# Optimization experiments

Hardware: AMD Instinct MI355X
Metric: run time of the kernel (lower is better)

## Reference

```python
import jax, jax.numpy as jnp
import numpy as np

OBS = 256      # observation_space_size == state_vector_len
SV = 2047      # STATE_VECTORS = WMG_MAX_OBS
D = 256        # tfm_vec_size = 8 heads * 32 head_size
H = 8
HD = 32
L = 2          # TFM_NUM_LAYERS
FF = 1024      # TFM_HIDDEN_SIZE
ACH = 512      # AC_HIDDEN_LAYER_SIZE
A = 16         # action_space_size


def setup_inputs() -> dict:
    key = jax.random.key(0)
    ks = jax.random.split(key, 24)
    r = lambda k, s: (jax.random.normal(k, s, jnp.float32) * 0.02)
    inp = {
        "observation": jax.random.normal(ks[0], (OBS,), jnp.float32),
        "old_vectors": jax.random.normal(ks[1], (SV, OBS), jnp.float32),
        "W_core": r(ks[2], (OBS, D)), "b_core": jnp.zeros((D,), jnp.float32),
        # memo embedding takes cat(state_vec, age_onehot) of size OBS+SV
        "W_memo": r(ks[3], (OBS + SV, D)), "b_memo": jnp.zeros((D,), jnp.float32),
        "Wq": r(ks[4], (L, D, D)), "bq": jnp.zeros((L, D), jnp.float32),
        "Wk": r(ks[5], (L, D, D)), "bk": jnp.zeros((L, D), jnp.float32),
        "Wv": r(ks[6], (L, D, D)), "bv": jnp.zeros((L, D), jnp.float32),
        "Wo": r(ks[7], (L, D, D)), "bo": jnp.zeros((L, D), jnp.float32),
        "ln1_g": jnp.ones((L, D), jnp.float32), "ln1_b": jnp.zeros((L, D), jnp.float32),
        "ln2_g": jnp.ones((L, D), jnp.float32), "ln2_b": jnp.zeros((L, D), jnp.float32),
        "W_ff1": r(ks[8], (L, D, FF)), "b_ff1": jnp.zeros((L, FF), jnp.float32),
        "W_ff2": r(ks[9], (L, FF, D)), "b_ff2": jnp.zeros((L, D), jnp.float32),
        "aW1": r(ks[10], (D, ACH)), "ab1": jnp.zeros((ACH,), jnp.float32),
        "aW2": r(ks[11], (ACH, ACH)), "ab2": jnp.zeros((ACH,), jnp.float32),
        "aWo": r(ks[12], (ACH, A)), "abo": jnp.zeros((A,), jnp.float32),
        "cW1": r(ks[13], (D, ACH)), "cb1": jnp.zeros((ACH,), jnp.float32),
        "cW2": r(ks[14], (ACH, ACH)), "cb2": jnp.zeros((ACH,), jnp.float32),
        "cWo": r(ks[15], (ACH, 1)), "cbo": jnp.zeros((1,), jnp.float32),
    }
    return inp


def _ln(x, g, b, eps=1e-5):
    m = jnp.mean(x, axis=-1, keepdims=True)
    v = jnp.mean(jnp.square(x - m), axis=-1, keepdims=True)
    return (x - m) * jax.lax.rsqrt(v + eps) * g + b


def reference(observation, old_vectors, W_core, b_core, W_memo, b_memo,
              Wq, bq, Wk, bk, Wv, bv, Wo, bo,
              ln1_g, ln1_b, ln2_g, ln2_b, W_ff1, b_ff1, W_ff2, b_ff2,
              aW1, ab1, aW2, ab2, aWo, abo, cW1, cb1, cW2, cb2, cWo, cbo):
    # core embedding [D]
    emb0 = observation @ W_core + b_core
    # fused memo + age-onehot embedding: cat(vec_i, e_i) @ W_memo == vec_i @ W_memo[:OBS] + W_memo[OBS+i]
    memo_emb = old_vectors @ W_memo[:OBS] + W_memo[OBS:] + b_memo  # [SV, D]
    x = jnp.concatenate([emb0[None, :], memo_emb], axis=0)[None]   # [1, 1+SV, D]
    S = 1 + SV
    scale = 1.0 / np.sqrt(HD).astype(np.float32)
    for l in range(L):
        q = (x @ Wq[l] + bq[l]).reshape(1, S, H, HD)
        k = (x @ Wk[l] + bk[l]).reshape(1, S, H, HD)
        v = (x @ Wv[l] + bv[l]).reshape(1, S, H, HD)
        scores = jnp.einsum('bqhd,bkhd->bhqk', q, k) * scale       # [1,H,S,S]
        probs = jax.nn.softmax(scores, axis=-1)
        ctx = jnp.einsum('bhqk,bkhd->bqhd', probs, v).reshape(1, S, D)
        x = _ln(x + ctx @ Wo[l] + bo[l], ln1_g[l], ln1_b[l])
        h = jax.nn.gelu(x @ W_ff1[l] + b_ff1[l])
        x = _ln(x + h @ W_ff2[l] + b_ff2[l], ln2_g[l], ln2_b[l])
    t = x[:, 0, :]                                                 # [1, D]
    ha = jnp.tanh(jnp.tanh(t @ aW1 + ab1) @ aW2 + ab2)
    policy = ha @ aWo + abo                                        # [1, A] logits
    hc = jnp.tanh(jnp.tanh(t @ cW1 + cb1) @ cW2 + cb2)
    value_est = hc @ cWo + cbo                                     # [1, 1]
    # WMG_MAX_MEMOS == 0 path: new state vector is tanh(observation)
    new_vector = jnp.tanh(observation)                             # [OBS]
    return value_est, policy, new_vector
```

## Files before the change

kernel.cpp:

```cpp
#include <hip/hip_runtime.h>
#include <stdint.h>

typedef __attribute__((ext_vector_type(8))) short bf16x8;
typedef __attribute__((ext_vector_type(4))) float f32x4;

constexpr int kSEQ = 2048;
constexpr int kD   = 256;
constexpr int kHD  = 32;
constexpr int kFF  = 1024;
constexpr int kACH = 512;
constexpr int kA   = 16;

__device__ __forceinline__ unsigned short f2b(float f) {
  union { float f; unsigned int u; } v; v.f = f;
  unsigned int r = v.u + 0x7FFFu + ((v.u >> 16) & 1u);
  return (unsigned short)(r >> 16);
}

struct ConvTable {
  const float* src[14];
  int K[14];
  int N[14];
  int dst[14];
  int tstart[15];
};

union SharedU {
  struct { unsigned short lt[64][72]; } cv;
  struct { unsigned short Al[64][40]; unsigned short Bl[32][40]; } g64;
  struct { unsigned short Kl[64][40]; unsigned short Vt[32][72];
           unsigned short Pl[4][16][72]; } at;
  struct { unsigned short As[16][264]; float2 red[4][16]; } lg;
  struct { float tl[512]; float red[4][64]; } hd;
  struct { float ha[512]; float hc[512]; float vred[4]; } h3;
};

struct MegaParams {
  ConvTable tab;
  const float *obs, *oldv, *Wcore, *bcore, *bmemo, *Wmemo2;
  const float *bq, *bk, *bv, *bo, *ln1g, *ln1b, *ln2g, *ln2b, *bff1, *bff2;
  const float *aW1, *ab1, *aW2, *ab2, *aWo, *abo;
  const float *cW1, *cb1, *cW2, *cb2, *cWo, *cbo;
  float* xf; unsigned short* xb;
  unsigned short *qb, *kb, *vb, *hb, *wT;
  float *pacc, *pml, *pf, *h1, *h2, *out;
  int oMemo, oQKV[2], oWoT[2], oFF1[2], oFF2[2];
  int convJobs, nsplit, tpb;
};

__device__ void ph_conv(const MegaParams& p, SharedU& sh) {
  const int tid = threadIdx.x;
  for (int job = blockIdx.x; job <= p.convJobs; job += gridDim.x) {
    __syncthreads();
    if (job == p.convJobs) {
      float a = p.bcore[tid];
      #pragma unroll 8
      for (int k = 0; k < 256; k++) a += p.obs[k] * p.Wcore[k * kD + tid];
      p.xf[tid] = a;
      p.xb[tid] = f2b(a);
      continue;
    }
    int m = 0;
    while (job >= p.tab.tstart[m + 1]) m++;
    const int tloc = job - p.tab.tstart[m];
    const int N = p.tab.N[m], K = p.tab.K[m];
    const int ntile = N >> 6;
    const int k0 = (tloc / ntile) * 64, n0 = (tloc % ntile) * 64;
    const float* src = p.tab.src[m];
    {
      const int r = tid >> 2, c16 = (tid & 3) * 16;
      const float* sp = src + (size_t)(k0 + r) * N + n0 + c16;
      #pragma unroll
      for (int j = 0; j < 16; j++) sh.cv.lt[r][c16 + j] = f2b(sp[j]);
    }
    __syncthreads();
    {
      const int n = tid >> 2, kc = (tid & 3) * 16;
      unsigned short* dp = p.wT + p.tab.dst[m] + (size_t)(n0 + n) * K + k0 + kc;
      unsigned short g[16];
      #pragma unroll
      for (int j = 0; j < 16; j++) g[j] = sh.cv.lt[kc + j][n];
      *(bf16x8*)dp = *(bf16x8*)&g[0];
      *(bf16x8*)(dp + 8) = *(bf16x8*)&g[8];
    }
  }
}

template <int EPI, bool AF32>
__device__ __forceinline__ void gemm_job(
    SharedU& sh, int m0, int n0, const void* Ap, int lda, int M, int Kloop,
    const unsigned short* BT, int ldb,
    const float* p0, const float* p1, const float* p2,
    void* o0, void* o1, void* o2) {
  const int tid = threadIdx.x;
  const int w = tid >> 6, l = tid & 63, lg = l >> 4, lr = l & 15;
  const int sr = tid >> 2, sk = (tid & 3) * 8;
  f32x4 acc[2];
  #pragma unroll
  for (int c = 0; c < 2; c++)
    #pragma unroll
    for (int i = 0; i < 4; i++) acc[c][i] = 0.f;

  auto loadA = [&](int k0) -> bf16x8 {
    bf16x8 av;
    if (m0 + sr < M) {
      if constexpr (AF32) {
        const float* ap = (const float*)Ap + (size_t)(m0 + sr) * lda + k0 + sk;
        #pragma unroll
        for (int j = 0; j < 8; j++) av[j] = (short)f2b(ap[j]);
      } else {
        av = *(const bf16x8*)((const unsigned short*)Ap +
                              (size_t)(m0 + sr) * lda + k0 + sk);
      }
    } else {
      #pragma unroll
      for (int j = 0; j < 8; j++) av[j] = 0;
    }
    return av;
  };

  bf16x8 av = loadA(0);
  bf16x8 bv;
  if (tid < 128) bv = *(const bf16x8*)(BT + (size_t)(n0 + sr) * ldb + sk);

  for (int k0 = 0; k0 < Kloop; k0 += 32) {
    __syncthreads();
    *(bf16x8*)&sh.g64.Al[sr][sk] = av;
    if (tid < 128) *(bf16x8*)&sh.g64.Bl[sr][sk] = bv;
    __syncthreads();
    if (k0 + 32 < Kloop) {
      av = loadA(k0 + 32);
      if (tid < 128)
        bv = *(const bf16x8*)(BT + (size_t)(n0 + sr) * ldb + k0 + 32 + sk);
    }
    bf16x8 af = *(bf16x8*)&sh.g64.Al[w * 16 + lr][8 * lg];
    #pragma unroll
    for (int c = 0; c < 2; c++) {
      bf16x8 bf = *(bf16x8*)&sh.g64.Bl[c * 16 + lr][8 * lg];
      acc[c] = __builtin_amdgcn_mfma_f32_16x16x32_bf16(af, bf, acc[c], 0, 0, 0);
    }
  }

  #pragma unroll
  for (int c = 0; c < 2; c++) {
    #pragma unroll
    for (int i = 0; i < 4; i++) {
      const int gr = m0 + w * 16 + 4 * lg + i;
      const int gc = n0 + c * 16 + lr;
      if (gr >= M) continue;
      float v = acc[c][i];
      if constexpr (EPI == 0) {
        v += p0[gc] + p1[(size_t)gr * kD + gc];
        ((float*)o0)[(size_t)(gr + 1) * kD + gc] = v;
        ((unsigned short*)o1)[(size_t)(gr + 1) * kD + gc] = f2b(v);
      } else if constexpr (EPI == 1) {
        const int t = gc >> 8, cc = gc & 255;
        const float* bp = (t == 0) ? p0 : (t == 1 ? p1 : p2);
        unsigned short* op = (t == 0) ? (unsigned short*)o0
                              : (t == 1 ? (unsigned short*)o1
                                        : (unsigned short*)o2);
        v += bp[cc];
        if (t == 0) v *= 0.17677669529663687f;
        op[(size_t)gr * kD + cc] = f2b(v);
      } else if constexpr (EPI == 2) {
        v += p0[gc];
        const float g =
            0.5f * v *
            (1.0f + tanhf(0.7978845608028654f * (v + 0.044715f * v * v * v)));
        ((unsigned short*)o0)[(size_t)gr * kFF + gc] = f2b(g);
      } else {
        ((float*)o0)[(size_t)gr * kD + gc] = v;
      }
    }
  }
}

template <int EPI, bool AF32>
__device__ void ph_gemm(SharedU& sh, const void* Ap, int lda, int M, int K,
                        const unsigned short* BT, int Mtiles, int Ntiles,
                        const float* p0, const float* p1, const float* p2,
                        void* o0, void* o1, void* o2) {
  const int njobs = Mtiles * Ntiles;
  for (int job = blockIdx.x; job < njobs; job += gridDim.x) {
    const int m0 = (job % Mtiles) * 64, n0 = (job / Mtiles) * 32;
    gemm_job<EPI, AF32>(sh, m0, n0, Ap, lda, M, K, BT, K, p0, p1, p2,
                        o0, o1, o2);
  }
}

__device__ void ph_ff2p(const MegaParams& p, SharedU& sh, int lyr) {
  for (int job = blockIdx.x; job < 1024; job += gridDim.x) {
    const int m0 = (job & 31) * 64;
    const int n0 = ((job >> 5) & 7) * 32;
    const int kc = (job >> 8) * 256;
    gemm_job<3, false>(sh, m0, n0, p.hb + kc, kFF, 2048, 256,
                       p.wT + p.oFF2[lyr] + kc, kFF,
                       nullptr, nullptr, nullptr,
                       p.pf + (size_t)(job >> 8) * kSEQ * kD, nullptr, nullptr);
  }
}

__device__ void attn_job(SharedU& sh, int qb_, int h, int s, int tpb,
                         const unsigned short* q, const unsigned short* k,
                         const unsigned short* v, float* pacc, float* pml) {
  const int tid = threadIdx.x;
  const int w = tid >> 6, l = tid & 63, lg = l >> 4, lr = l & 15;
  const int q0 = qb_ * 64;
  const int hoff = h * kHD;
  const int sr = tid >> 2, sk = (tid & 3) * 8;
  const int t0 = s * tpb;

  const bf16x8 qf =
      *(const bf16x8*)(q + (size_t)(q0 + w * 16 + lr) * kD + hoff + 8 * lg);

  float m_[4], l_[4];
  f32x4 acc[2];
  #pragma unroll
  for (int i = 0; i < 4; i++) { m_[i] = -1e30f; l_[i] = 0.f; }
  #pragma unroll
  for (int dt = 0; dt < 2; dt++)
    #pragma unroll
    for (int i = 0; i < 4; i++) acc[dt][i] = 0.f;

  bf16x8 kreg = *(const bf16x8*)(k + (size_t)(t0 * 64 + sr) * kD + hoff + sk);
  bf16x8 vreg = *(const bf16x8*)(v + (size_t)(t0 * 64 + sr) * kD + hoff + sk);

  for (int t = 0; t < tpb; t++) {
    __syncthreads();
    *(bf16x8*)&sh.at.Kl[sr][sk] = kreg;
    #pragma unroll
    for (int j = 0; j < 8; j++) sh.at.Vt[sk + j][sr] = (unsigned short)vreg[j];
    __syncthreads();
    if (t + 1 < tpb) {
      const size_t nx = (size_t)((t0 + t + 1) * 64 + sr) * kD + hoff + sk;
      kreg = *(const bf16x8*)(k + nx);
      vreg = *(const bf16x8*)(v + nx);
    }
    f32x4 sc[4];
    #pragma unroll
    for (int c = 0; c < 4; c++) {
      f32x4 z;
      #pragma unroll
      for (int i = 0; i < 4; i++) z[i] = 0.f;
      bf16x8 kf = *(bf16x8*)&sh.at.Kl[c * 16 + lr][8 * lg];
      sc[c] = __builtin_amdgcn_mfma_f32_16x16x32_bf16(qf, kf, z, 0, 0, 0);
    }
    float tm[4];
    #pragma unroll
    for (int i = 0; i < 4; i++)
      tm[i] = fmaxf(fmaxf(sc[0][i], sc[1][i]), fmaxf(sc[2][i], sc[3][i]));
    #pragma unroll
    for (int mm = 1; mm <= 8; mm <<= 1)
      #pragma unroll
      for (int i = 0; i < 4; i++) tm[i] = fmaxf(tm[i], __shfl_xor(tm[i], mm));
    float pv[4][4], rs[4], corr[4];
    #pragma unroll
    for (int i = 0; i < 4; i++) {
      const float nm = fmaxf(m_[i], tm[i]);
      corr[i] = __expf(m_[i] - nm);
      m_[i] = nm;
      rs[i] = 0.f;
    }
    #pragma unroll
    for (int c = 0; c < 4; c++)
      #pragma unroll
      for (int i = 0; i < 4; i++) {
        pv[c][i] = __expf(sc[c][i] - m_[i]);
        rs[i] += pv[c][i];
      }
    #pragma unroll
    for (int mm = 1; mm <= 8; mm <<= 1)
      #pragma unroll
      for (int i = 0; i < 4; i++) rs[i] += __shfl_xor(rs[i], mm);
    #pragma unroll
    for (int i = 0; i < 4; i++) {
      l_[i] = l_[i] * corr[i] + rs[i];
      acc[0][i] *= corr[i];
      acc[1][i] *= corr[i];
    }
    #pragma unroll
    for (int c = 0; c < 4; c++)
      #pragma unroll
      for (int i = 0; i < 4; i++)
        sh.at.Pl[w][4 * lg + i][c * 16 + lr] = f2b(pv[c][i]);
    __syncthreads();
    #pragma unroll
    for (int k2 = 0; k2 < 2; k2++) {
      bf16x8 pf_ = *(bf16x8*)&sh.at.Pl[w][lr][k2 * 32 + 8 * lg];
      #pragma unroll
      for (int dt = 0; dt < 2; dt++) {
        bf16x8 vf = *(bf16x8*)&sh.at.Vt[dt * 16 + lr][k2 * 32 + 8 * lg];
        acc[dt] = __builtin_amdgcn_mfma_f32_16x16x32_bf16(pf_, vf, acc[dt], 0, 0, 0);
      }
    }
  }

  const int pb = s * 8 + h;
  float* pa = pacc + (size_t)pb * kSEQ * kHD;
  float* pm = pml + (size_t)pb * kSEQ * 2;
  #pragma unroll
  for (int dt = 0; dt < 2; dt++)
    #pragma unroll
    for (int i = 0; i < 4; i++) {
      const int gr = q0 + w * 16 + 4 * lg + i;
      pa[(size_t)gr * kHD + dt * 16 + lr] = acc[dt][i];
    }
  if (lr == 0) {
    #pragma unroll
    for (int i = 0; i < 4; i++) {
      const int gr = q0 + w * 16 + 4 * lg + i;
      float2 ml; ml.x = m_[i]; ml.y = l_[i];
      *(float2*)&pm[(size_t)gr * 2] = ml;
    }
  }
}

__device__ void ph_attn(const MegaParams& p, SharedU& sh) {
  const int njobs = 256 * p.nsplit;
  for (int job = blockIdx.x; job < njobs; job += gridDim.x) {
    const int qb_ = job & 31, h = (job >> 5) & 7, s = job >> 8;
    attn_job(sh, qb_, h, s, p.tpb, p.qb, p.kb, p.vb, p.pacc, p.pml);
  }
}

__device__ __forceinline__ void ln_write(SharedU& sh, float vloc[4][4], int r0,
                                         const float* gam, const float* bet,
                                         float* xf, unsigned short* xb) {
  const int tid = threadIdx.x;
  const int w = tid >> 6, l = tid & 63, lg = l >> 4, lr = l & 15;
  float ps[4], ps2[4];
  #pragma unroll
  for (int i = 0; i < 4; i++) {
    ps[i] = 0.f; ps2[i] = 0.f;
    #pragma unroll
    for (int c = 0; c < 4; c++) {
      ps[i] += vloc[c][i];
      ps2[i] += vloc[c][i] * vloc[c][i];
    }
  }
  #pragma unroll
  for (int mm = 1; mm <= 8; mm <<= 1)
    #pragma unroll
    for (int i = 0; i < 4; i++) {
      ps[i] += __shfl_xor(ps[i], mm);
      ps2[i] += __shfl_xor(ps2[i], mm);
    }
  if (lr == 0) {
    #pragma unroll
    for (int i = 0; i < 4; i++) {
      float2 t; t.x = ps[i]; t.y = ps2[i];
      sh.lg.red[w][4 * lg + i] = t;
    }
  }
  __syncthreads();
  #pragma unroll
  for (int i = 0; i < 4; i++) {
    const int ri = 4 * lg + i;
    float sx = 0.f, sx2 = 0.f;
    #pragma unroll
    for (int ww = 0; ww < 4; ww++) {
      float2 t = sh.lg.red[ww][ri];
      sx += t.x; sx2 += t.y;
    }
    const float mean = sx * (1.0f / 256.0f);
    const float var = sx2 * (1.0f / 256.0f) - mean * mean;
    const float rstd = rsqrtf(var + 1e-5f);
    const int gr = r0 + ri;
    #pragma unroll
    for (int c = 0; c < 4; c++) {
      const int col = w * 64 + c * 16 + lr;
      const float y = (vloc[c][i] - mean) * rstd * gam[col] + bet[col];
      xf[(size_t)gr * kD + col] = y;
      xb[(size_t)gr * kD + col] = f2b(y);
    }
  }
}

__device__ void ph_woln(const MegaParams& p, SharedU& sh, int lyr) {
  const unsigned short* BT = p.wT + p.oWoT[lyr];
  const float* bias = p.bo + lyr * kD;
  const float* gam = p.ln1g + lyr * kD;
  const float* bet = p.ln1b + lyr * kD;
  const int tid = threadIdx.x;
  const int w = tid >> 6, l = tid & 63, lg = l >> 4, lr = l & 15;
  for (int job = blockIdx.x; job < 128; job += gridDim.x) {
    const int r0 = job * 16;
    __syncthreads();
    {
      const int row = r0 + (tid >> 4);
      const int kc = (tid & 15) * 16;
      const int h_ = kc >> 5;
      float mx = -1e30f;
      for (int s2 = 0; s2 < p.nsplit; s2++)
        mx = fmaxf(mx, p.pml[((size_t)(s2 * 8 + h_) * kSEQ + row) * 2]);
      float L = 0.f;
      const int d0 = kc & 31;
      float o[16];
      #pragma unroll
      for (int j = 0; j < 16; j++) o[j] = 0.f;
      for (int s2 = 0; s2 < p.nsplit; s2++) {
        const size_t pb = (size_t)(s2 * 8 + h_) * kSEQ + row;
        const float2 t = *(const float2*)&p.pml[pb * 2];
        const float es = __expf(t.x - mx);
        L += t.y * es;
        const float* pa = p.pacc + pb * kHD + d0;
        #pragma unroll
        for (int j = 0; j < 16; j++) o[j] += pa[j] * es;
      }
      const float inv = 1.0f / L;
      unsigned short* dst = &sh.lg.As[tid >> 4][kc];
      #pragma unroll
      for (int j = 0; j < 16; j++) dst[j] = f2b(o[j] * inv);
    }
    __syncthreads();
    f32x4 acc[4];
    #pragma unroll
    for (int c = 0; c < 4; c++)
      #pragma unroll
      for (int i = 0; i < 4; i++) acc[c][i] = 0.f;
    #pragma unroll 2
    for (int k0 = 0; k0 < 256; k0 += 32) {
      bf16x8 af = *(bf16x8*)&sh.lg.As[lr][k0 + 8 * lg];
      #pragma unroll
      for (int c = 0; c < 4; c++) {
        bf16x8 bf = *(const bf16x8*)(BT + (size_t)(w * 64 + c * 16 + lr) * 256 +
                                     k0 + 8 * lg);
        acc[c] = __builtin_amdgcn_mfma_f32_16x16x32_bf16(af, bf, acc[c], 0, 0, 0);
      }
    }
    float vloc[4][4];
    #pragma unroll
    for (int c = 0; c < 4; c++)
      #pragma unroll
      for (int i = 0; i < 4; i++) {
        const int col = w * 64 + c * 16 + lr;
        const int gr = r0 + 4 * lg + i;
        vloc[c][i] = acc[c][i] + bias[col] + p.xf[(size_t)gr * kD + col];
      }
    ln_write(sh, vloc, r0, gam, bet, p.xf, p.xb);
  }
}

__device__ void ph_ln2r(const MegaParams& p, int lyr) {
  const float* bias = p.bff2 + lyr * kD;
  const float* gam = p.ln2g + lyr * kD;
  const float* bet = p.ln2b + lyr * kD;
  const int w = threadIdx.x >> 6, l = threadIdx.x & 63;
  const int row = blockIdx.x * 4 + w;
  f32x4 v = *(const f32x4*)(p.xf + (size_t)row * kD + l * 4);
  f32x4 b4 = *(const f32x4*)(bias + l * 4);
  #pragma unroll
  for (int i = 0; i < 4; i++) v[i] += b4[i];
  #pragma unroll
  for (int s = 0; s < 4; s++) {
    f32x4 t = *(const f32x4*)(p.pf + ((size_t)s * kSEQ + row) * kD + l * 4);
    #pragma unroll
    for (int i = 0; i < 4; i++) v[i] += t[i];
  }
  float su = v[0] + v[1] + v[2] + v[3];
  #pragma unroll
  for (int mm = 1; mm < 64; mm <<= 1) su += __shfl_xor(su, mm);
  const float mn = su * (1.0f / 256.0f);
  const float d0 = v[0] - mn, d1 = v[1] - mn, d2 = v[2] - mn, d3 = v[3] - mn;
  float s2 = d0 * d0 + d1 * d1 + d2 * d2 + d3 * d3;
  #pragma unroll
  for (int mm = 1; mm < 64; mm <<= 1) s2 += __shfl_xor(s2, mm);
  const float rstd = rsqrtf(s2 * (1.0f / 256.0f) + 1e-5f);
  f32x4 g4 = *(const f32x4*)(gam + l * 4);
  f32x4 be4 = *(const f32x4*)(bet + l * 4);
  f32x4 y;
  y[0] = d0 * rstd * g4[0] + be4[0];
  y[1] = d1 * rstd * g4[1] + be4[1];
  y[2] = d2 * rstd * g4[2] + be4[2];
  y[3] = d3 * rstd * g4[3] + be4[3];
  *(f32x4*)(p.xf + (size_t)row * kD + l * 4) = y;
  unsigned long long pk = (unsigned long long)f2b(y[0]) |
                          ((unsigned long long)f2b(y[1]) << 16) |
                          ((unsigned long long)f2b(y[2]) << 32) |
                          ((unsigned long long)f2b(y[3]) << 48);
  *(unsigned long long*)(p.xb + (size_t)row * kD + l * 4) = pk;
}

__device__ void ph_h1(const MegaParams& p, SharedU& sh) {
  const int tid = threadIdx.x;
  for (int job = blockIdx.x; job < 16; job += gridDim.x) {
    __syncthreads();
    sh.hd.tl[tid] = p.xf[tid];
    __syncthreads();
    const int jj = job * 64;
    const bool actor = jj < 512;
    const float* W = actor ? p.aW1 : p.cW1;
    const float* b = actor ? p.ab1 : p.cb1;
    const int j0 = actor ? jj : jj - 512;
    const int ks = tid >> 6, j = tid & 63;
    float s = 0.f;
    #pragma unroll 4
    for (int k2 = ks * 64; k2 < ks * 64 + 64; k2++)
      s += sh.hd.tl[k2] * W[(size_t)k2 * kACH + j0 + j];
    sh.hd.red[ks][j] = s;
    __syncthreads();
    if (tid < 64) {
      float t = sh.hd.red[0][tid] + sh.hd.red[1][tid] + sh.hd.red[2][tid] +
                sh.hd.red[3][tid] + b[j0 + tid];
      p.h1[jj + tid] = tanhf(t);
    }
  }
}

__device__ void ph_h2(const MegaParams& p, SharedU& sh) {
  const int tid = threadIdx.x;
  for (int job = blockIdx.x; job < 16; job += gridDim.x) {
    __syncthreads();
    const int jj = job * 64;
    const bool actor = jj < 512;
    const float* hin = actor ? p.h1 : p.h1 + 512;
    sh.hd.tl[tid] = hin[tid];
    sh.hd.tl[tid + 256] = hin[tid + 256];
    __syncthreads();
    const float* W = actor ? p.aW2 : p.cW2;
    const float* b = actor ? p.ab2 : p.cb2;
    const int j0 = actor ? jj : jj - 512;
    const int ks = tid >> 6, j = tid & 63;
    float s = 0.f;
    #pragma unroll 4
    for (int k2 = ks * 128; k2 < ks * 128 + 128; k2++)
      s += sh.hd.tl[k2] * W[(size_t)k2 * kACH + j0 + j];
    sh.hd.red[ks][j] = s;
    __syncthreads();
    if (tid < 64) {
      float t = sh.hd.red[0][tid] + sh.hd.red[1][tid] + sh.hd.red[2][tid] +
                sh.hd.red[3][tid] + b[j0 + tid];
      p.h2[jj + tid] = tanhf(t);
    }
  }
}

__device__ void ph_h3(const MegaParams& p, SharedU& sh) {
  const int tid = threadIdx.x;
  for (int job = blockIdx.x; job < 1; job += gridDim.x) {
    __syncthreads();
    sh.h3.ha[tid] = p.h2[tid];
    sh.h3.ha[tid + 256] = p.h2[tid + 256];
    sh.h3.hc[tid] = p.h2[512 + tid];
    sh.h3.hc[tid + 256] = p.h2[768 + tid];
    __syncthreads();
    const int g = tid >> 4, lane16 = tid & 15;
    float s = 0.f;
    for (int k2 = lane16 * 32; k2 < lane16 * 32 + 32; k2++)
      s += sh.h3.ha[k2] * p.aWo[(size_t)k2 * kA + g];
    #pragma unroll
    for (int mm = 1; mm <= 8; mm <<= 1) s += __shfl_xor(s, mm);
    if (lane16 == 0) p.out[1 + g] = s + p.abo[g];
    float vv = sh.h3.hc[tid] * p.cWo[tid] + sh.h3.hc[tid + 256] * p.cWo[tid + 256];
    #pragma unroll
    for (int mm = 1; mm <= 32; mm <<= 1) vv += __shfl_xor(vv, mm);
    if ((tid & 63) == 0) sh.h3.vred[tid >> 6] = vv;
    __syncthreads();
    if (tid == 0)
      p.out[0] = sh.h3.vred[0] + sh.h3.vred[1] + sh.h3.vred[2] + sh.h3.vred[3] +
                 p.cbo[0];
    p.out[17 + tid] = tanhf(p.obs[tid]);
  }
}

__global__ __launch_bounds__(256) void k_conv(MegaParams p) { __shared__ SharedU sh; ph_conv(p, sh); }
__global__ __launch_bounds__(256) void k_memo(MegaParams p) {
  __shared__ SharedU sh;
  ph_gemm<0, true>(sh, p.oldv, 256, 2047, 256, p.wT + p.oMemo, 32, 8,
                   p.bmemo, p.Wmemo2, nullptr, p.xf, p.xb, nullptr);
}
__global__ __launch_bounds__(256) void k_qkv(MegaParams p, int lyr) {
  __shared__ SharedU sh;
  ph_gemm<1, false>(sh, p.xb, 256, 2048, 256, p.wT + p.oQKV[lyr], 32, 24,
                    p.bq + lyr * 256, p.bk + lyr * 256, p.bv + lyr * 256,
                    p.qb, p.kb, p.vb);
}
__global__ __launch_bounds__(256) void k_attn(MegaParams p) { __shared__ SharedU sh; ph_attn(p, sh); }
__global__ __launch_bounds__(256) void k_woln(MegaParams p, int lyr) { __shared__ SharedU sh; ph_woln(p, sh, lyr); }
__global__ __launch_bounds__(256) void k_ff1(MegaParams p, int lyr) {
  __shared__ SharedU sh;
  ph_gemm<2, false>(sh, p.xb, 256, 2048, 256, p.wT + p.oFF1[lyr], 32, 32,
                    p.bff1 + lyr * 1024, nullptr, nullptr, p.hb, nullptr, nullptr);
}
__global__ __launch_bounds__(256) void k_ff2p(MegaParams p, int lyr) { __shared__ SharedU sh; ph_ff2p(p, sh, lyr); }
__global__ __launch_bounds__(256) void k_ln2r(MegaParams p, int lyr) { ph_ln2r(p, lyr); }
__global__ __launch_bounds__(256) void k_h1(MegaParams p) { __shared__ SharedU sh; ph_h1(p, sh); }
__global__ __launch_bounds__(256) void k_h2(MegaParams p) { __shared__ SharedU sh; ph_h2(p, sh); }
__global__ __launch_bounds__(256) void k_h3(MegaParams p) { __shared__ SharedU sh; ph_h3(p, sh); }

extern "C" void kernel_launch(void* const* d_in, const int* in_sizes, int n_in,
                              void* d_out, int out_size, void* d_ws, size_t ws_size,
                              hipStream_t stream) {
  const float* obs   = (const float*)d_in[0];
  const float* oldv  = (const float*)d_in[1];
  const float* Wcore = (const float*)d_in[2];
  const float* bcore = (const float*)d_in[3];
  const float* Wmemo = (const float*)d_in[4];
  const float* bmemo = (const float*)d_in[5];
  const float* Wq    = (const float*)d_in[6];
  const float* bq    = (const float*)d_in[7];
  const float* Wk    = (const float*)d_in[8];
  const float* bk    = (const float*)d_in[9];
  const float* Wv    = (const float*)d_in[10];
  const float* bv    = (const float*)d_in[11];
  const float* Wo    = (const float*)d_in[12];
  const float* bo    = (const float*)d_in[13];
  const float* ln1g  = (const float*)d_in[14];
  const float* ln1b  = (const float*)d_in[15];
  const float* ln2g  = (const float*)d_in[16];
  const float* ln2b  = (const float*)d_in[17];
  const float* Wff1  = (const float*)d_in[18];
  const float* bff1  = (const float*)d_in[19];
  const float* Wff2  = (const float*)d_in[20];
  const float* bff2  = (const float*)d_in[21];

  MegaParams P;
  P.obs = obs; P.oldv = oldv; P.Wcore = Wcore; P.bcore = bcore;
  P.bmemo = bmemo; P.Wmemo2 = Wmemo + 256 * 256;
  P.bq = bq; P.bk = bk; P.bv = bv; P.bo = bo;
  P.ln1g = ln1g; P.ln1b = ln1b; P.ln2g = ln2g; P.ln2b = ln2b;
  P.bff1 = bff1; P.bff2 = bff2;
  P.aW1 = (const float*)d_in[22]; P.ab1 = (const float*)d_in[23];
  P.aW2 = (const float*)d_in[24]; P.ab2 = (const float*)d_in[25];
  P.aWo = (const float*)d_in[26]; P.abo = (const float*)d_in[27];
  P.cW1 = (const float*)d_in[28]; P.cb1 = (const float*)d_in[29];
  P.cW2 = (const float*)d_in[30]; P.cb2 = (const float*)d_in[31];
  P.cWo = (const float*)d_in[32]; P.cbo = (const float*)d_in[33];

  char* ws = (char*)d_ws;
  P.xf = (float*)(ws + 0);
  P.xb = (unsigned short*)(ws + (2u << 20));
  P.qb = (unsigned short*)(ws + (3u << 20));
  P.kb = (unsigned short*)(ws + (4u << 20));
  P.vb = (unsigned short*)(ws + (5u << 20));
  P.hb = (unsigned short*)(ws + (6u << 20));
  P.h1 = (float*)(ws + (10u << 20));
  P.h2 = (float*)(ws + (10u << 20) + 8192);
  P.wT = (unsigned short*)(ws + (10u << 20) + 65536);
  P.out = (float*)d_out;

  int nsplit = 8;
  const size_t paccOff = (size_t)14u << 20;
  const size_t pmlOff  = (size_t)31u << 20;
  const size_t pfOff   = (size_t)33u << 20;
  while (nsplit > 1 &&
         (paccOff + (size_t)nsplit * 8 * kSEQ * kHD * 4 > pmlOff ||
          pfOff + (size_t)4 * kSEQ * kD * 4 > ws_size))
    nsplit >>= 1;
  P.pacc = (float*)(ws + paccOff);
  P.pml  = (float*)(ws + pmlOff);
  P.pf   = (float*)(ws + pfOff);
  P.nsplit = nsplit;
  P.tpb = 32 / nsplit;

  P.oMemo = 0;
  int cur = 65536;
  for (int l2 = 0; l2 < 2; l2++) {
    P.oQKV[l2] = cur; cur += 196608;
    P.oWoT[l2] = cur; cur += 65536;
    P.oFF1[l2] = cur; cur += 262144;
    P.oFF2[l2] = cur; cur += 262144;
  }

  int idx = 0, ts = 0;
  auto add = [&](const float* s, int K, int N, int dst) {
    P.tab.src[idx] = s; P.tab.K[idx] = K; P.tab.N[idx] = N;
    P.tab.dst[idx] = dst; P.tab.tstart[idx] = ts;
    ts += (K >> 6) * (N >> 6); idx++;
  };
  add(Wmemo, 256, 256, P.oMemo);
  for (int l2 = 0; l2 < 2; l2++) {
    add(Wq + l2 * 65536, 256, 256, P.oQKV[l2]);
    add(Wk + l2 * 65536, 256, 256, P.oQKV[l2] + 65536);
    add(Wv + l2 * 65536, 256, 256, P.oQKV[l2] + 131072);
    add(Wo + l2 * 65536, 256, 256, P.oWoT[l2]);
    add(Wff1 + l2 * 262144, 256, 1024, P.oFF1[l2]);
    add(Wff2 + l2 * 262144, 1024, 256, P.oFF2[l2]);
  }
  P.tab.tstart[idx] = ts;
  P.convJobs = ts;

  k_conv<<<ts + 1, 256, 0, stream>>>(P);
  k_memo<<<256, 256, 0, stream>>>(P);
  for (int lyr = 0; lyr < 2; lyr++) {
    k_qkv<<<768, 256, 0, stream>>>(P, lyr);
    k_attn<<<256 * nsplit, 256, 0, stream>>>(P);
    k_woln<<<128, 256, 0, stream>>>(P, lyr);
    k_ff1<<<1024, 256, 0, stream>>>(P, lyr);
    k_ff2p<<<1024, 256, 0, stream>>>(P, lyr);
    k_ln2r<<<512, 256, 0, stream>>>(P, lyr);
  }
  k_h1<<<16, 256, 0, stream>>>(P);
  k_h2<<<16, 256, 0, stream>>>(P);
  k_h3<<<1, 256, 0, stream>>>(P);
}
```

Measured before the change: 207.3 us.

## Fuse weight conversion with memo GEMM and fold actor-critic heads into final LN

The memo embedding GEMM now reads the fp32 Wmemo directly and transposes it into LDS, so it no longer depends on a converted copy. That lets it run in the same launch as the weight conversion for the remaining matrices. The three actor/critic head kernels are folded into block 0 of the last LayerNorm kernel, which removes four kernel launches in total. The cost is that a single block runs the serial head MLPs, and the row-wise head now has to read the first token row produced in that same block.

New measurement: 236.5 us. 1.14x slower.

```diff
diff --git a/kernel.cpp b/kernel.cpp
--- a/kernel.cpp
+++ b/kernel.cpp
@@ -8,7 +8,6 @@
 constexpr int kD   = 256;
 constexpr int kHD  = 32;
 constexpr int kFF  = 1024;
-constexpr int kACH = 512;
 constexpr int kA   = 16;
 
 __device__ __forceinline__ unsigned short f2b(float f) {
@@ -18,11 +17,11 @@
 }
 
 struct ConvTable {
-  const float* src[14];
-  int K[14];
-  int N[14];
-  int dst[14];
-  int tstart[15];
+  const float* src[13];
+  int K[13];
+  int N[13];
+  int dst[13];
+  int tstart[14];
 };
 
 union SharedU {
@@ -31,64 +30,130 @@
   struct { unsigned short Kl[64][40]; unsigned short Vt[32][72];
            unsigned short Pl[4][16][72]; } at;
   struct { unsigned short As[16][264]; float2 red[4][16]; } lg;
-  struct { float tl[512]; float red[4][64]; } hd;
-  struct { float ha[512]; float hc[512]; float vred[4]; } h3;
 };
 
 struct MegaParams {
   ConvTable tab;
-  const float *obs, *oldv, *Wcore, *bcore, *bmemo, *Wmemo2;
+  const float *obs, *oldv, *Wcore, *bcore, *Wmemo0, *bmemo, *Wmemo2;
   const float *bq, *bk, *bv, *bo, *ln1g, *ln1b, *ln2g, *ln2b, *bff1, *bff2;
   const float *aW1, *ab1, *aW2, *ab2, *aWo, *abo;
   const float *cW1, *cb1, *cW2, *cb2, *cWo, *cbo;
   float* xf; unsigned short* xb;
   unsigned short *qb, *kb, *vb, *hb, *wT;
-  float *pacc, *pml, *pf, *h1, *h2, *out;
-  int oMemo, oQKV[2], oWoT[2], oFF1[2], oFF2[2];
+  float *pacc, *pml, *pf, *out;
+  int oQKV[2], oWoT[2], oFF1[2], oFF2[2];
   int convJobs, nsplit, tpb;
 };
 
-__device__ void ph_conv(const MegaParams& p, SharedU& sh) {
+__device__ void conv_job(const MegaParams& p, SharedU& sh, int job) {
   const int tid = threadIdx.x;
-  for (int job = blockIdx.x; job <= p.convJobs; job += gridDim.x) {
-    __syncthreads();
-    if (job == p.convJobs) {
-      float a = p.bcore[tid];
-      #pragma unroll 8
-      for (int k = 0; k < 256; k++) a += p.obs[k] * p.Wcore[k * kD + tid];
-      p.xf[tid] = a;
-      p.xb[tid] = f2b(a);
-      continue;
-    }
-    int m = 0;
-    while (job >= p.tab.tstart[m + 1]) m++;
-    const int tloc = job - p.tab.tstart[m];
-    const int N = p.tab.N[m], K = p.tab.K[m];
-    const int ntile = N >> 6;
-    const int k0 = (tloc / ntile) * 64, n0 = (tloc % ntile) * 64;
-    const float* src = p.tab.src[m];
-    {
-      const int r = tid >> 2, c16 = (tid & 3) * 16;
-      const float* sp = src + (size_t)(k0 + r) * N + n0 + c16;
-      #pragma unroll
-      for (int j = 0; j < 16; j++) sh.cv.lt[r][c16 + j] = f2b(sp[j]);
-    }
-    __syncthreads();
-    {
-      const int n = tid >> 2, kc = (tid & 3) * 16;
-      unsigned short* dp = p.wT + p.tab.dst[m] + (size_t)(n0 + n) * K + k0 + kc;
-      unsigned short g[16];
-      #pragma unroll
-      for (int j = 0; j < 16; j++) g[j] = sh.cv.lt[kc + j][n];
-      *(bf16x8*)dp = *(bf16x8*)&g[0];
-      *(bf16x8*)(dp + 8) = *(bf16x8*)&g[8];
-    }
-  }
-}
-
-template <int EPI, bool AF32>
+  if (job == p.convJobs) {
+    float a = p.bcore[tid];
+    #pragma unroll 8
+    for (int k = 0; k < 256; k++) a += p.obs[k] * p.Wcore[k * kD + tid];
+    p.xf[tid] = a;
+    p.xb[tid] = f2b(a);
+    return;
+  }
+  int m = 0;
+  while (job >= p.tab.tstart[m + 1]) m++;
+  const int tloc = job - p.tab.tstart[m];
+  const int N = p.tab.N[m], K = p.tab.K[m];
+  const int ntile = N >> 6;
+  const int k0 = (tloc / ntile) * 64, n0 = (tloc % ntile) * 64;
+  const float* src = p.tab.src[m];
+  {
+    const int r = tid >> 2, c16 = (tid & 3) * 16;
+    const float* sp = src + (size_t)(k0 + r) * N + n0 + c16;
+    #pragma unroll
+    for (int j = 0; j < 16; j++) sh.cv.lt[r][c16 + j] = f2b(sp[j]);
+  }
+  __syncthreads();
+  {
+    const int n = tid >> 2, kc = (tid & 3) * 16;
+    unsigned short* dp = p.wT + p.tab.dst[m] + (size_t)(n0 + n) * K + k0 + kc;
+    unsigned short g[16];
+    #pragma unroll
+    for (int j = 0; j < 16; j++) g[j] = sh.cv.lt[kc + j][n];
+    *(bf16x8*)dp = *(bf16x8*)&g[0];
+    *(bf16x8*)(dp + 8) = *(bf16x8*)&g[8];
+  }
+}
+
+__device__ void memo_job(const MegaParams& p, SharedU& sh, int job) {
+  const int tid = threadIdx.x;
+  const int w = tid >> 6, l = tid & 63, lg = l >> 4, lr = l & 15;
+  const int sr = tid >> 2, sk = (tid & 3) * 8;
+  const int kr = tid >> 3, nc = (tid & 7) * 4;
+  const int m0 = (job & 31) * 64, n0 = (job >> 5) * 32;
+  f32x4 acc[2];
+  #pragma unroll
+  for (int c = 0; c < 2; c++)
+    #pragma unroll
+    for (int i = 0; i < 4; i++) acc[c][i] = 0.f;
+
+  auto loadA = [&](int k0) -> bf16x8 {
+    bf16x8 av;
+    if (m0 + sr < 2047) {
+      const float* ap = p.oldv + (size_t)(m0 + sr) * 256 + k0 + sk;
+      #pragma unroll
+      for (int j = 0; j < 8; j++) av[j] = (short)f2b(ap[j]);
+    } else {
+      #pragma unroll
+      for (int j = 0; j < 8; j++) av[j] = 0;
+    }
+    return av;
+  };
+  auto loadB = [&](int k0, float* b4) {
+    const float* bp = p.Wmemo0 + (size_t)(k0 + kr) * kD + n0 + nc;
+    #pragma unroll
+    for (int j = 0; j < 4; j++) b4[j] = bp[j];
+  };
+
+  bf16x8 av = loadA(0);
+  float b4[4];
+  loadB(0, b4);
+
+  for (int k0 = 0; k0 < 256; k0 += 32) {
+    __syncthreads();
+    *(bf16x8*)&sh.g64.Al[sr][sk] = av;
+    #pragma unroll
+    for (int j = 0; j < 4; j++) sh.g64.Bl[nc + j][kr] = f2b(b4[j]);
+    __syncthreads();
+    if (k0 + 32 < 256) {
+      av = loadA(k0 + 32);
+      loadB(k0 + 32, b4);
+    }
+    bf16x8 af = *(bf16x8*)&sh.g64.Al[w * 16 + lr][8 * lg];
+    #pragma unroll
+    for (int c = 0; c < 2; c++) {
+      bf16x8 bf = *(bf16x8*)&sh.g64.Bl[c * 16 + lr][8 * lg];
+      acc[c] = __builtin_amdgcn_mfma_f32_16x16x32_bf16(af, bf, acc[c], 0, 0, 0);
+    }
+  }
+
+  #pragma unroll
+  for (int c = 0; c < 2; c++)
+    #pragma unroll
+    for (int i = 0; i < 4; i++) {
+      const int gr = m0 + w * 16 + 4 * lg + i;
+      const int gc = n0 + c * 16 + lr;
+      if (gr >= 2047) continue;
+      const float v = acc[c][i] + p.bmemo[gc] + p.Wmemo2[(size_t)gr * kD + gc];
+      p.xf[(size_t)(gr + 1) * kD + gc] = v;
+      p.xb[(size_t)(gr + 1) * kD + gc] = f2b(v);
+    }
+}
+
+__global__ __launch_bounds__(256) void k_cvm(MegaParams p) {
+  __shared__ SharedU sh;
+  if (blockIdx.x < 256) memo_job(p, sh, blockIdx.x);
+  else conv_job(p, sh, blockIdx.x - 256);
+}
+
+template <int EPI>
 __device__ __forceinline__ void gemm_job(
-    SharedU& sh, int m0, int n0, const void* Ap, int lda, int M, int Kloop,
+    SharedU& sh, int m0, int n0, const unsigned short* Ap, int lda, int Kloop,
     const unsigned short* BT, int ldb,
     const float* p0, const float* p1, const float* p2,
     void* o0, void* o1, void* o2) {
@@ -101,25 +166,7 @@
     #pragma unroll
     for (int i = 0; i < 4; i++) acc[c][i] = 0.f;
 
-  auto loadA = [&](int k0) -> bf16x8 {
-    bf16x8 av;
-    if (m0 + sr < M) {
-      if constexpr (AF32) {
-        const float* ap = (const float*)Ap + (size_t)(m0 + sr) * lda + k0 + sk;
-        #pragma unroll
-        for (int j = 0; j < 8; j++) av[j] = (short)f2b(ap[j]);
-      } else {
-        av = *(const bf16x8*)((const unsigned short*)Ap +
-                              (size_t)(m0 + sr) * lda + k0 + sk);
-      }
-    } else {
-      #pragma unroll
-      for (int j = 0; j < 8; j++) av[j] = 0;
-    }
-    return av;
-  };
-
-  bf16x8 av = loadA(0);
+  bf16x8 av = *(const bf16x8*)(Ap + (size_t)(m0 + sr) * lda + sk);
   bf16x8 bv;
   if (tid < 128) bv = *(const bf16x8*)(BT + (size_t)(n0 + sr) * ldb + sk);
 
@@ -129,7 +176,7 @@
     if (tid < 128) *(bf16x8*)&sh.g64.Bl[sr][sk] = bv;
     __syncthreads();
     if (k0 + 32 < Kloop) {
-      av = loadA(k0 + 32);
+      av = *(const bf16x8*)(Ap + (size_t)(m0 + sr) * lda + k0 + 32 + sk);
       if (tid < 128)
         bv = *(const bf16x8*)(BT + (size_t)(n0 + sr) * ldb + k0 + 32 + sk);
     }
@@ -147,13 +194,8 @@
     for (int i = 0; i < 4; i++) {
       const int gr = m0 + w * 16 + 4 * lg + i;
       const int gc = n0 + c * 16 + lr;
-      if (gr >= M) continue;
       float v = acc[c][i];
-      if constexpr (EPI == 0) {
-        v += p0[gc] + p1[(size_t)gr * kD + gc];
-        ((float*)o0)[(size_t)(gr + 1) * kD + gc] = v;
-        ((unsigned short*)o1)[(size_t)(gr + 1) * kD + gc] = f2b(v);
-      } else if constexpr (EPI == 1) {
+      if constexpr (EPI == 1) {
         const int t = gc >> 8, cc = gc & 255;
         const float* bp = (t == 0) ? p0 : (t == 1 ? p1 : p2);
         unsigned short* op = (t == 0) ? (unsigned short*)o0
@@ -175,28 +217,34 @@
   }
 }
 
-template <int EPI, bool AF32>
-__device__ void ph_gemm(SharedU& sh, const void* Ap, int lda, int M, int K,
-                        const unsigned short* BT, int Mtiles, int Ntiles,
-                        const float* p0, const float* p1, const float* p2,
-                        void* o0, void* o1, void* o2) {
-  const int njobs = Mtiles * Ntiles;
-  for (int job = blockIdx.x; job < njobs; job += gridDim.x) {
-    const int m0 = (job % Mtiles) * 64, n0 = (job / Mtiles) * 32;
-    gemm_job<EPI, AF32>(sh, m0, n0, Ap, lda, M, K, BT, K, p0, p1, p2,
-                        o0, o1, o2);
-  }
-}
-
-__device__ void ph_ff2p(const MegaParams& p, SharedU& sh, int lyr) {
+__global__ __launch_bounds__(256) void k_qkv(MegaParams p, int lyr) {
+  __shared__ SharedU sh;
+  for (int job = blockIdx.x; job < 768; job += gridDim.x) {
+    const int m0 = (job & 31) * 64, n0 = (job >> 5) * 32;
+    gemm_job<1>(sh, m0, n0, p.xb, 256, 256, p.wT + p.oQKV[lyr], 256,
+                p.bq + lyr * 256, p.bk + lyr * 256, p.bv + lyr * 256,
+                p.qb, p.kb, p.vb);
+  }
+}
+
+__global__ __launch_bounds__(256) void k_ff1(MegaParams p, int lyr) {
+  __shared__ SharedU sh;
+  for (int job = blockIdx.x; job < 1024; job += gridDim.x) {
+    const int m0 = (job & 31) * 64, n0 = (job >> 5) * 32;
+    gemm_job<2>(sh, m0, n0, p.xb, 256, 256, p.wT + p.oFF1[lyr], 256,
+                p.bff1 + lyr * 1024, nullptr, nullptr, p.hb, nullptr, nullptr);
+  }
+}
+
+__global__ __launch_bounds__(256) void k_ff2p(MegaParams p, int lyr) {
+  __shared__ SharedU sh;
   for (int job = blockIdx.x; job < 1024; job += gridDim.x) {
     const int m0 = (job & 31) * 64;
     const int n0 = ((job >> 5) & 7) * 32;
     const int kc = (job >> 8) * 256;
-    gemm_job<3, false>(sh, m0, n0, p.hb + kc, kFF, 2048, 256,
-                       p.wT + p.oFF2[lyr] + kc, kFF,
-                       nullptr, nullptr, nullptr,
-                       p.pf + (size_t)(job >> 8) * kSEQ * kD, nullptr, nullptr);
+    gemm_job<3>(sh, m0, n0, p.hb + kc, kFF, 256,
+                p.wT + p.oFF2[lyr] + kc, kFF, nullptr, nullptr, nullptr,
+                p.pf + (size_t)(job >> 8) * kSEQ * kD, nullptr, nullptr);
   }
 }
 
@@ -315,7 +363,8 @@
   }
 }
 
-__device__ void ph_attn(const MegaParams& p, SharedU& sh) {
+__global__ __launch_bounds__(256) void k_attn(MegaParams p) {
+  __shared__ SharedU sh;
   const int njobs = 256 * p.nsplit;
   for (int job = blockIdx.x; job < njobs; job += gridDim.x) {
     const int qb_ = job & 31, h = (job >> 5) & 7, s = job >> 8;
@@ -376,7 +425,8 @@
   }
 }
 
-__device__ void ph_woln(const MegaParams& p, SharedU& sh, int lyr) {
+__global__ __launch_bounds__(256) void k_woln(MegaParams p, int lyr) {
+  __shared__ SharedU sh;
   const unsigned short* BT = p.wT + p.oWoT[lyr];
   const float* bias = p.bo + lyr * kD;
   const float* gam = p.ln1g + lyr * kD;
@@ -441,11 +491,17 @@
   }
 }
 
-__device__ void ph_ln2r(const MegaParams& p, int lyr) {
+template <bool WH>
+__global__ __launch_bounds__(256) void k_ln2r(MegaParams p, int lyr) {
+  __shared__ float tl[256];
+  __shared__ float hA[1024];
+  __shared__ float hB[1024];
+  __shared__ float vred[4];
   const float* bias = p.bff2 + lyr * kD;
   const float* gam = p.ln2g + lyr * kD;
   const float* bet = p.ln2b + lyr * kD;
-  const int w = threadIdx.x >> 6, l = threadIdx.x & 63;
+  const int tid = threadIdx.x;
+  const int w = tid >> 6, l = tid & 63;
   const int row = blockIdx.x * 4 + w;
   f32x4 v = *(const f32x4*)(p.xf + (size_t)row * kD + l * 4);
   f32x4 b4 = *(const f32x4*)(bias + l * 4);
@@ -479,114 +535,53 @@
                           ((unsigned long long)f2b(y[2]) << 32) |
                           ((unsigned long long)f2b(y[3]) << 48);
   *(unsigned long long*)(p.xb + (size_t)row * kD + l * 4) = pk;
-}
-
-__device__ void ph_h1(const MegaParams& p, SharedU& sh) {
-  const int tid = threadIdx.x;
-  for (int job = blockIdx.x; job < 16; job += gridDim.x) {
-    __syncthreads();
-    sh.hd.tl[tid] = p.xf[tid];
-    __syncthreads();
-    const int jj = job * 64;
-    const bool actor = jj < 512;
-    const float* W = actor ? p.aW1 : p.cW1;
-    const float* b = actor ? p.ab1 : p.cb1;
-    const int j0 = actor ? jj : jj - 512;
-    const int ks = tid >> 6, j = tid & 63;
-    float s = 0.f;
-    #pragma unroll 4
-    for (int k2 = ks * 64; k2 < ks * 64 + 64; k2++)
-      s += sh.hd.tl[k2] * W[(size_t)k2 * kACH + j0 + j];
-    sh.hd.red[ks][j] = s;
-    __syncthreads();
-    if (tid < 64) {
-      float t = sh.hd.red[0][tid] + sh.hd.red[1][tid] + sh.hd.red[2][tid] +
-                sh.hd.red[3][tid] + b[j0 + tid];
-      p.h1[jj + tid] = tanhf(t);
-    }
-  }
-}
-
-__device__ void ph_h2(const MegaParams& p, SharedU& sh) {
-  const int tid = threadIdx.x;
-  for (int job = blockIdx.x; job < 16; job += gridDim.x) {
-    __syncthreads();
-    const int jj = job * 64;
-    const bool actor = jj < 512;
-    const float* hin = actor ? p.h1 : p.h1 + 512;
-    sh.hd.tl[tid] = hin[tid];
-    sh.hd.tl[tid + 256] = hin[tid + 256];
-    __syncthreads();
-    const float* W = actor ? p.aW2 : p.cW2;
-    const float* b = actor ? p.ab2 : p.cb2;
-    const int j0 = actor ? jj : jj - 512;
-    const int ks = tid >> 6, j = tid & 63;
-    float s = 0.f;
-    #pragma unroll 4
-    for (int k2 = ks * 128; k2 < ks * 128 + 128; k2++)
-      s += sh.hd.tl[k2] * W[(size_t)k2 * kACH + j0 + j];
-    sh.hd.red[ks][j] = s;
-    __syncthreads();
-    if (tid < 64) {
-      float t = sh.hd.red[0][tid] + sh.hd.red[1][tid] + sh.hd.red[2][tid] +
-                sh.hd.red[3][tid] + b[j0 + tid];
-      p.h2[jj + tid] = tanhf(t);
-    }
-  }
-}
-
-__device__ void ph_h3(const MegaParams& p, SharedU& sh) {
-  const int tid = threadIdx.x;
-  for (int job = blockIdx.x; job < 1; job += gridDim.x) {
-    __syncthreads();
-    sh.h3.ha[tid] = p.h2[tid];
-    sh.h3.ha[tid + 256] = p.h2[tid + 256];
-    sh.h3.hc[tid] = p.h2[512 + tid];
-    sh.h3.hc[tid + 256] = p.h2[768 + tid];
-    __syncthreads();
-    const int g = tid >> 4, lane16 = tid & 15;
-    float s = 0.f;
-    for (int k2 = lane16 * 32; k2 < lane16 * 32 + 32; k2++)
-      s += sh.h3.ha[k2] * p.aWo[(size_t)k2 * kA + g];
-    #pragma unroll
-    for (int mm = 1; mm <= 8; mm <<= 1) s += __shfl_xor(s, mm);
-    if (lane16 == 0) p.out[1 + g] = s + p.abo[g];
-    float vv = sh.h3.hc[tid] * p.cWo[tid] + sh.h3.hc[tid + 256] * p.cWo[tid + 256];
-    #pragma unroll
-    for (int mm = 1; mm <= 32; mm <<= 1) vv += __shfl_xor(vv, mm);
-    if ((tid & 63) == 0) sh.h3.vred[tid >> 6] = vv;
-    __syncthreads();
-    if (tid == 0)
-      p.out[0] = sh.h3.vred[0] + sh.h3.vred[1] + sh.h3.vred[2] + sh.h3.vred[3] +
-                 p.cbo[0];
-    p.out[17 + tid] = tanhf(p.obs[tid]);
-  }
-}
-
-__global__ __launch_bounds__(256) void k_conv(MegaParams p) { __shared__ SharedU sh; ph_conv(p, sh); }
-__global__ __launch_bounds__(256) void k_memo(MegaParams p) {
-  __shared__ SharedU sh;
-  ph_gemm<0, true>(sh, p.oldv, 256, 2047, 256, p.wT + p.oMemo, 32, 8,
-                   p.bmemo, p.Wmemo2, nullptr, p.xf, p.xb, nullptr);
-}
-__global__ __launch_bounds__(256) void k_qkv(MegaParams p, int lyr) {
-  __shared__ SharedU sh;
-  ph_gemm<1, false>(sh, p.xb, 256, 2048, 256, p.wT + p.oQKV[lyr], 32, 24,
-                    p.bq + lyr * 256, p.bk + lyr * 256, p.bv + lyr * 256,
-                    p.qb, p.kb, p.vb);
-}
-__global__ __launch_bounds__(256) void k_attn(MegaParams p) { __shared__ SharedU sh; ph_attn(p, sh); }
-__global__ __launch_bounds__(256) void k_woln(MegaParams p, int lyr) { __shared__ SharedU sh; ph_woln(p, sh, lyr); }
-__global__ __launch_bounds__(256) void k_ff1(MegaParams p, int lyr) {
-  __shared__ SharedU sh;
-  ph_gemm<2, false>(sh, p.xb, 256, 2048, 256, p.wT + p.oFF1[lyr], 32, 32,
-                    p.bff1 + lyr * 1024, nullptr, nullptr, p.hb, nullptr, nullptr);
-}
-__global__ __launch_bounds__(256) void k_ff2p(MegaParams p, int lyr) { __shared__ SharedU sh; ph_ff2p(p, sh, lyr); }
-__global__ __launch_bounds__(256) void k_ln2r(MegaParams p, int lyr) { ph_ln2r(p, lyr); }
-__global__ __launch_bounds__(256) void k_h1(MegaParams p) { __shared__ SharedU sh; ph_h1(p, sh); }
-__global__ __launch_bounds__(256) void k_h2(MegaParams p) { __shared__ SharedU sh; ph_h2(p, sh); }
-__global__ __launch_bounds__(256) void k_h3(MegaParams p) { __shared__ SharedU sh; ph_h3(p, sh); }
+
+  if constexpr (WH) {
+    if (blockIdx.x == 0) {
+      if (w == 0) *(f32x4*)&tl[l * 4] = y;
+      __syncthreads();
+      float a0 = p.ab1[tid], a1 = p.ab1[tid + 256];
+      float c0 = p.cb1[tid], c1 = p.cb1[tid + 256];
+      for (int k = 0; k < 256; k++) {
+        const float x = tl[k];
+        a0 += x * p.aW1[(size_t)k * 512 + tid];
+        a1 += x * p.aW1[(size_t)k * 512 + tid + 256];
+        c0 += x * p.cW1[(size_t)k * 512 + tid];
+        c1 += x * p.cW1[(size_t)k * 512 + tid + 256];
+      }
+      hA[tid] = tanhf(a0); hA[tid + 256] = tanhf(a1);
+      hA[512 + tid] = tanhf(c0); hA[768 + tid] = tanhf(c1);
+      __syncthreads();
+      float b0 = p.ab2[tid], b1 = p.ab2[tid + 256];
+      float e0 = p.cb2[tid], e1 = p.cb2[tid + 256];
+      for (int k = 0; k < 512; k++) {
+        const float xa = hA[k], xc = hA[512 + k];
+        b0 += xa * p.aW2[(size_t)k * 512 + tid];
+        b1 += xa * p.aW2[(size_t)k * 512 + tid + 256];
+        e0 += xc * p.cW2[(size_t)k * 512 + tid];
+        e1 += xc * p.cW2[(size_t)k * 512 + tid + 256];
+      }
+      hB[tid] = tanhf(b0); hB[tid + 256] = tanhf(b1);
+      hB[512 + tid] = tanhf(e0); hB[768 + tid] = tanhf(e1);
+      __syncthreads();
+      const int g = tid >> 4, l16 = tid & 15;
+      float s = 0.f;
+      for (int k2 = l16 * 32; k2 < l16 * 32 + 32; k2++)
+        s += hB[k2] * p.aWo[(size_t)k2 * kA + g];
+      #pragma unroll
+      for (int mm = 1; mm <= 8; mm <<= 1) s += __shfl_xor(s, mm);
+      if (l16 == 0) p.out[1 + g] = s + p.abo[g];
+      float vv = hB[512 + tid] * p.cWo[tid] + hB[768 + tid] * p.cWo[tid + 256];
+      #pragma unroll
+      for (int mm = 1; mm <= 32; mm <<= 1) vv += __shfl_xor(vv, mm);
+      if ((tid & 63) == 0) vred[tid >> 6] = vv;
+      __syncthreads();
+      if (tid == 0)
+        p.out[0] = vred[0] + vred[1] + vred[2] + vred[3] + p.cbo[0];
+      p.out[17 + tid] = tanhf(p.obs[tid]);
+    }
+  }
+}
 
 extern "C" void kernel_launch(void* const* d_in, const int* in_sizes, int n_in,
                               void* d_out, int out_size, void* d_ws, size_t ws_size,
@@ -616,7 +611,7 @@
 
   MegaParams P;
   P.obs = obs; P.oldv = oldv; P.Wcore = Wcore; P.bcore = bcore;
-  P.bmemo = bmemo; P.Wmemo2 = Wmemo + 256 * 256;
+  P.Wmemo0 = Wmemo; P.bmemo = bmemo; P.Wmemo2 = Wmemo + 256 * 256;
   P.bq = bq; P.bk = bk; P.bv = bv; P.bo = bo;
   P.ln1g = ln1g; P.ln1b = ln1b; P.ln2g = ln2g; P.ln2b = ln2b;
   P.bff1 = bff1; P.bff2 = bff2;
@@ -634,9 +629,7 @@
   P.kb = (unsigned short*)(ws + (4u << 20));
   P.vb = (unsigned short*)(ws + (5u << 20));
   P.hb = (unsigned short*)(ws + (6u << 20));
-  P.h1 = (float*)(ws + (10u << 20));
-  P.h2 = (float*)(ws + (10u << 20) + 8192);
-  P.wT = (unsigned short*)(ws + (10u << 20) + 65536);
+  P.wT = (unsigned short*)(ws + (10u << 20));
   P.out = (float*)d_out;
 
   int nsplit = 8;
@@ -653,8 +646,7 @@
   P.nsplit = nsplit;
   P.tpb = 32 / nsplit;
 
-  P.oMemo = 0;
-  int cur = 65536;
+  int cur = 0;
   for (int l2 = 0; l2 < 2; l2++) {
     P.oQKV[l2] = cur; cur += 196608;
     P.oWoT[l2] = cur; cur += 65536;
@@ -668,7 +660,6 @@
     P.tab.dst[idx] = dst; P.tab.tstart[idx] = ts;
     ts += (K >> 6) * (N >> 6); idx++;
   };
-  add(Wmemo, 256, 256, P.oMemo);
   for (int l2 = 0; l2 < 2; l2++) {
     add(Wq + l2 * 65536, 256, 256, P.oQKV[l2]);
     add(Wk + l2 * 65536, 256, 256, P.oQKV[l2] + 65536);
@@ -680,17 +671,14 @@
   P.tab.tstart[idx] = ts;
   P.convJobs = ts;
 
-  k_conv<<<ts + 1, 256, 0, stream>>>(P);
-  k_memo<<<256, 256, 0, stream>>>(P);
+  k_cvm<<<256 + ts + 1, 256, 0, stream>>>(P);
   for (int lyr = 0; lyr < 2; lyr++) {
     k_qkv<<<768, 256, 0, stream>>>(P, lyr);
     k_attn<<<256 * nsplit, 256, 0, stream>>>(P);
     k_woln<<<128, 256, 0, stream>>>(P, lyr);
     k_ff1<<<1024, 256, 0, stream>>>(P, lyr);
     k_ff2p<<<1024, 256, 0, stream>>>(P, lyr);
-    k_ln2r<<<512, 256, 0, stream>>>(P, lyr);
-  }
-  k_h1<<<16, 256, 0, stream>>>(P);
-  k_h2<<<16, 256, 0, stream>>>(P);
-  k_h3<<<1, 256, 0, stream>>>(P);
-}
+    if (lyr == 0) k_ln2r<false><<<512, 256, 0, stream>>>(P, lyr);
+    else          k_ln2r<true><<<512, 256, 0, stream>>>(P, lyr);
+  }
+}
```
